# Optimization experiments

Measured on AMD Instinct MI355X. Metric: run time of the kernel, lower is better.

## Reference

```python
import jax, jax.numpy as jnp
import numpy as np

N_QUBITS = 12
N_LAYERS = 3
HID = 16
IN_DIM = 6
BATCH = 4096
C64 = jnp.complex64


def _ry(t):
    c = jnp.cos(t / 2).astype(C64)
    s = jnp.sin(t / 2).astype(C64)
    return jnp.stack([jnp.stack([c, -s], -1), jnp.stack([s, c], -1)], -2)


def _rx(t):
    c = jnp.cos(t / 2).astype(C64)
    s = jnp.sin(t / 2).astype(C64)
    js = 1j * s
    return jnp.stack([jnp.stack([c, -js], -1), jnp.stack([-js, c], -1)], -2)


def _rz(t):
    e = jnp.exp(-1j * t.astype(C64) / 2)
    z = jnp.zeros_like(e)
    return jnp.stack([jnp.stack([e, z], -1), jnp.stack([z, jnp.conj(e)], -1)], -2)


def _apply_1q(state, U, wire):
    # state: (B,) + (2,)*n ; U: (2,2) shared or (B,2,2) per-sample
    s = jnp.moveaxis(state, wire + 1, 1)
    if U.ndim == 2:
        s = jnp.einsum('ij,bj...->bi...', U, s)
    else:
        s = jnp.einsum('bij,bj...->bi...', U, s)
    return jnp.moveaxis(s, 1, wire + 1)


def _cnot(state, c, t):
    ax_c = c + 1
    s0 = jnp.take(state, 0, axis=ax_c)
    s1 = jnp.take(state, 1, axis=ax_c)
    t_ax = t + 1 if t < c else t  # target axis after removing control axis
    s1 = jnp.flip(s1, axis=t_ax)  # X on target when control=1
    return jnp.stack([s0, s1], axis=ax_c)


def _quantum(angles, qparams):
    # angles: (B, n_qubits) angle-encoding RY rotations; qparams: (L, n, 3)
    B = angles.shape[0]
    n = N_QUBITS
    state = jnp.zeros((B,) + (2,) * n, C64).at[(slice(None),) + (0,) * n].set(1.0)
    for i in range(n):
        state = _apply_1q(state, _ry(angles[:, i]), i)
    for l in range(N_LAYERS):
        for i in range(n):
            # RX then RY then RZ on wire i -> fused 2x2
            U = _rz(qparams[l, i, 2]) @ _ry(qparams[l, i, 1]) @ _rx(qparams[l, i, 0])
            state = _apply_1q(state, U, i)
        for i in range(n - 1):
            state = _cnot(state, i, i + 1)
        if n > 2:
            state = _cnot(state, n - 1, 0)
    p = state.real ** 2 + state.imag ** 2  # (B,) + (2,)*n
    evs = []
    for i in range(n):
        axes = tuple(a for a in range(1, n + 1) if a != i + 1)
        pi = p.sum(axes)  # (B, 2)
        evs.append(pi[:, 0] - pi[:, 1])
    return jnp.stack(evs, axis=1)  # (B, n) PauliZ expvals


def setup_inputs() -> dict:
    key = jax.random.key(0)
    ks = jax.random.split(key, 14)
    w = lambda k, shape: jax.random.normal(k, shape, jnp.float32) * 0.1
    return {
        'x': jax.random.normal(ks[0], (BATCH, IN_DIM), jnp.float32),
        'W1': w(ks[1], (HID, IN_DIM)), 'b1': w(ks[2], (HID,)),
        'W2': w(ks[3], (HID, HID)), 'b2': w(ks[4], (HID,)),
        'W3': w(ks[5], (N_QUBITS, HID)), 'b3': w(ks[6], (N_QUBITS,)),
        'qparams': w(ks[7], (N_LAYERS, N_QUBITS, 3)),
        'P1': w(ks[8], (HID, N_QUBITS)), 'c1': w(ks[9], (HID,)),
        'P2': w(ks[10], (8, HID)), 'c2': w(ks[11], (8,)),
        'P3': w(ks[12], (1, 8)), 'c3': w(ks[13], (1,)),
    }


def reference(x, W1, b1, W2, b2, W3, b3, qparams, P1, c1, P2, c2, P3, c3):
    # classical preprocessor (dropout = identity at inference)
    h = jax.nn.relu(x @ W1.T + b1)
    h = jax.nn.relu(h @ W2.T + b2)
    angles = h @ W3.T + b3  # (B, n_qubits)
    q = _quantum(angles, qparams)  # (B, n_qubits)
    # classical postprocessor
    o = jax.nn.relu(q @ P1.T + c1)
    o = jax.nn.relu(o @ P2.T + c2)
    o = jax.nn.sigmoid(o @ P3.T + c3)
    return o.squeeze(-1)  # (B,)
```

## Files before the change

kernel.cpp:

```cpp
#include <hip/hip_runtime.h>
#include <stdint.h>

#define NQ   12
#define DIM  4096
#define TPB  256

typedef float   v2f   __attribute__((ext_vector_type(2)));
typedef float   v4f   __attribute__((ext_vector_type(4)));
typedef float   f32x4 __attribute__((ext_vector_type(4)));
typedef _Float16 v2h  __attribute__((ext_vector_type(2)));
typedef _Float16 f16x8 __attribute__((ext_vector_type(8)));
typedef uint32_t u32x4 __attribute__((ext_vector_type(4)));

struct PassP {
  uint16_t v[4];
  uint16_t m[4];
  uint16_t td[4];
  uint8_t  np[8];
  uint8_t  wire[4];
  uint8_t  layer;
  uint8_t  pad[3];
};
struct ROC {
  uint16_t mask[12];
  uint8_t  bin[12];
};

constexpr int chbit(uint32_t x) { int b = -1; for (int i = 0; i < 32; ++i) if ((x >> i) & 1u) b = i; return b; }

constexpr void bmm(uint32_t* C, const uint32_t* A, const uint32_t* B) {
  for (int i = 0; i < NQ; ++i) {
    uint32_t r = 0;
    for (int j = 0; j < NQ; ++j) if ((A[i] >> j) & 1u) r ^= B[j];
    C[i] = r;
  }
}
constexpr void binv(const uint32_t* M, uint32_t* Inv) {
  uint32_t A[NQ] = {}, I[NQ] = {};
  for (int i = 0; i < NQ; ++i) { A[i] = M[i]; I[i] = 1u << i; }
  for (int c = 0; c < NQ; ++c) {
    int piv = -1;
    for (int r = c; r < NQ; ++r) if ((A[r] >> c) & 1u) { piv = r; break; }
    if (piv < 0) continue;
    uint32_t ta = A[c]; A[c] = A[piv]; A[piv] = ta;
    uint32_t ti = I[c]; I[c] = I[piv]; I[piv] = ti;
    for (int r = 0; r < NQ; ++r)
      if (r != c && ((A[r] >> c) & 1u)) { A[r] ^= A[c]; I[r] ^= I[c]; }
  }
  for (int i = 0; i < NQ; ++i) Inv[i] = I[i];
}

constexpr int rank5(const uint32_t* cols, int n) {
  uint32_t rows[5] = {}; int rnk = 0;
  for (int q = 0; q < n; ++q) {
    uint32_t x = cols[q] & 31u;
    for (int bit = 4; bit >= 0; --bit) {
      if (!((x >> bit) & 1u)) continue;
      if (rows[bit]) { x ^= rows[bit]; }
      else { rows[bit] = x; ++rnk; break; }
    }
  }
  return rnk;
}
constexpr int penalty(int r) {
  return r >= 5 ? 0 : r == 4 ? 58 : r == 3 ? 194 : r == 2 ? 469 : 1100;
}

constexpr PassP make_pass(int p) {
  PassP pp{};
  uint32_t A[NQ] = {}; A[0] = 0xFFEu;
  for (int i = 1; i < NQ; ++i) A[i] = (1u << (i + 1)) - 1u;
  uint32_t A2[NQ] = {}, Ai[NQ] = {}, A2i[NQ] = {};
  bmm(A2, A, A);
  binv(A, Ai); binv(A2, A2i);

  const int L = (p < 3) ? 1 : 2;
  const int wb = (p % 3) * 4;
  const uint32_t* M  = (L == 1) ? A  : A2;
  const uint32_t* Mi = (L == 1) ? Ai : A2i;
  uint32_t v0[4] = {}, m0[4] = {};
  for (int i = 0; i < 4; ++i) {
    int w = wb + i; uint32_t col = 0;
    for (int r = 0; r < NQ; ++r) col |= ((Mi[r] >> w) & 1u) << r;
    v0[i] = col; m0[i] = M[w];
  }
  uint32_t Bc[NQ] = {};
  for (int b = 0; b < NQ; ++b) {
    uint32_t col = 1u << b;
    for (int i = 0; i < 4; ++i) if ((m0[i] >> b) & 1u) col ^= v0[i];
    Bc[b] = col;
  }
  uint32_t redv[4] = {}; int pbit[4] = {}; uint32_t pivmask = 0;
  for (int i = 0; i < 4; ++i) {
    redv[i] = v0[i];
    for (int k2 = 0; k2 < i; ++k2) if ((redv[i] >> pbit[k2]) & 1u) redv[i] ^= redv[k2];
    pbit[i] = chbit(redv[i]); pivmask |= 1u << pbit[i];
  }
  uint8_t np0[8] = {}; int nc = 0;
  for (int b = 0; b < NQ; ++b) if (!((pivmask >> b) & 1u)) np0[nc++] = (uint8_t)b;

  int bestCost = 1 << 30;
  int bsel[4] = {0, 1, 2, 3}; int bperm[4] = {0, 1, 2, 3};
  for (int a = 0; a < 8; ++a) for (int b = a + 1; b < 8; ++b)
  for (int c = b + 1; c < 8; ++c) for (int d = c + 1; d < 8; ++d) {
    uint32_t jc[4] = {Bc[np0[a]], Bc[np0[b]], Bc[np0[c]], Bc[np0[d]]};
    int prk[4][4] = {};
    for (int i = 0; i < 4; ++i)
      for (int j = i + 1; j < 4; ++j) {
        uint32_t sp[6] = {jc[0], jc[1], jc[2], jc[3], v0[i], v0[j]};
        prk[i][j] = prk[j][i] = rank5(sp, 6);
      }
    for (int pa = 0; pa < 4; ++pa) for (int pb2 = 0; pb2 < 4; ++pb2) {
      if (pb2 == pa) continue;
      for (int pc = 0; pc < 4; ++pc) {
        if (pc == pa || pc == pb2) continue;
        const int pd = 6 - pa - pb2 - pc;
        const int cost = penalty(prk[pc][pd]) + penalty(prk[pb2][pc]);
        if (cost < bestCost) {
          bestCost = cost;
          bsel[0] = a; bsel[1] = b; bsel[2] = c; bsel[3] = d;
          bperm[0] = pa; bperm[1] = pb2; bperm[2] = pc; bperm[3] = pd;
        }
      }
    }
  }
  int rem[4] = {}; int rc2 = 0;
  for (int q = 0; q < 8; ++q)
    if (q != bsel[0] && q != bsel[1] && q != bsel[2] && q != bsel[3]) rem[rc2++] = q;

  uint8_t npn[8] = {};
  npn[0] = np0[bsel[0]]; npn[1] = np0[bsel[1]];
  npn[2] = np0[bsel[2]]; npn[3] = np0[bsel[3]];
  npn[4] = np0[rem[0]]; npn[5] = np0[rem[1]];
  npn[6] = np0[rem[2]]; npn[7] = np0[rem[3]];
  for (int q = 0; q < 8; ++q) pp.np[q] = npn[q];
  for (int i = 0; i < 4; ++i) {
    pp.v[i] = (uint16_t)v0[bperm[i]];
    pp.m[i] = (uint16_t)m0[bperm[i]];
    pp.wire[i] = (uint8_t)(wb + bperm[i]);
  }
  pp.td[0] = 0;
  pp.td[1] = (uint16_t)Bc[npn[4]];
  pp.td[2] = (uint16_t)Bc[npn[5]];
  pp.td[3] = (uint16_t)(Bc[npn[4]] ^ Bc[npn[5]]);
  pp.layer = (uint8_t)L;
  return pp;
}

constexpr PassP kp0 = make_pass(0);
constexpr PassP kp1 = make_pass(1);
constexpr PassP kp2 = make_pass(2);
constexpr PassP kp3 = make_pass(3);
constexpr PassP kp4 = make_pass(4);
constexpr PassP kp5 = make_pass(5);

template<int P>
constexpr PassP pget() {
  if constexpr (P == 0) return kp0;
  else if constexpr (P == 1) return kp1;
  else if constexpr (P == 2) return kp2;
  else if constexpr (P == 3) return kp3;
  else if constexpr (P == 4) return kp4;
  else return kp5;
}

constexpr ROC make_ro() {
  ROC r{};
  uint32_t A[NQ] = {}; A[0] = 0xFFEu;
  for (int i = 1; i < NQ; ++i) A[i] = (1u << (i + 1)) - 1u;
  uint32_t A2[NQ] = {}, A3[NQ] = {};
  bmm(A2, A, A); bmm(A3, A2, A);
  for (int i = 0; i < NQ; ++i) r.mask[i] = (uint16_t)A3[i];
  for (int i = 0; i < NQ; ++i) {
    uint32_t b = 0;
    b |= (uint32_t)(__builtin_popcount(A3[i] & (uint32_t)kp5.v[0]) & 1) << 0;
    b |= (uint32_t)(__builtin_popcount(A3[i] & (uint32_t)kp5.v[3]) & 1) << 1;
    b |= (uint32_t)(__builtin_popcount(A3[i] & (uint32_t)kp5.td[1]) & 1) << 2;
    b |= (uint32_t)(__builtin_popcount(A3[i] & (uint32_t)kp5.td[2]) & 1) << 3;
    r.bin[i] = (uint8_t)b;
  }
  return r;
}
constexpr ROC roc = make_ro();

__device__ __forceinline__ v2f cmulf(v2f a, v2f b) {
  return (v2f){a.x * b.x - a.y * b.y, a.x * b.y + a.y * b.x};
}
__device__ __forceinline__ uint32_t f2h2(float a, float b) {
  return __builtin_bit_cast(uint32_t, __builtin_amdgcn_cvt_pkrtz(a, b));
}
__device__ __forceinline__ uint32_t pk_rtn(float a, float b) {
  v2h h = {(_Float16)a, (_Float16)b};
  return __builtin_bit_cast(uint32_t, h);
}

__device__ __forceinline__ void build_u(const float* __restrict__ qp, int l, int w, float U[8]) {
  float p0 = qp[(l * 12 + w) * 3 + 0];
  float p1 = qp[(l * 12 + w) * 3 + 1];
  float p2 = qp[(l * 12 + w) * 3 + 2];
  float cx, sx, cy, sy, cz, sz;
  sincosf(0.5f * p0, &sx, &cx);
  sincosf(0.5f * p1, &sy, &cy);
  sincosf(0.5f * p2, &sz, &cz);
  float M00x =  cy * cx, M00y =  sy * sx;
  float M01x = -sy * cx, M01y = -cy * sx;
  float M10x =  sy * cx, M10y = -cy * sx;
  float M11x =  cy * cx, M11y = -sy * sx;
  U[0] = cz * M00x + sz * M00y; U[1] = cz * M00y - sz * M00x;
  U[2] = cz * M01x + sz * M01y; U[3] = cz * M01y - sz * M01x;
  U[4] = cz * M10x - sz * M10y; U[5] = cz * M10y + sz * M10x;
  U[6] = cz * M11x - sz * M11y; U[7] = cz * M11y + sz * M11x;
}

__device__ __forceinline__ int am_col(int c, int i) {
  return ((((c >> 2) ^ ((i >> 1) & 3)) << 2) | (c & 3));
}

template<int P>
__device__ __forceinline__ void build_am(uint32_t (*Am2)[32][16],
                                         const v2f (*gg)[12][4], int t) {
  constexpr PassP pp = pget<P>();
  const int r_ = t >> 4, c_ = t & 15;
  v2f e = (v2f){1.f, 0.f};
  #pragma unroll
  for (int i = 0; i < 4; ++i) {
    v2f u = gg[pp.layer - 1][pp.wire[i]][(((r_ >> i) & 1) << 1) | ((c_ >> i) & 1)];
    e = cmulf(e, u);
  }
  const int ra = 2 * r_, rb = 2 * r_ + 1;
  Am2[P & 1][ra][am_col(c_, ra)] = pk_rtn(e.x, -e.y);
  Am2[P & 1][rb][am_col(c_, rb)] = pk_rtn(e.y, e.x);
}

template<int P, bool LAST>
__device__ __forceinline__ void do_pass(uint32_t* st, uint32_t (*Am2)[32][16],
                                        const v2f (*gg)[12][4], int t, float* ev) {
  constexpr PassP pp = pget<P>();
  const int lane = t & 63;
  const int wv   = t >> 6;
  const int g    = lane >> 4;
  f16x8 a0, a1;
  {
    const int li = lane & 15;
    const int q0 = g ^ ((li >> 1) & 3);
    a0 = __builtin_bit_cast(f16x8, *reinterpret_cast<const u32x4*>(&Am2[P & 1][li][q0 * 4]));
    const int i1 = 16 + li;
    const int q1 = g ^ ((i1 >> 1) & 3);
    a1 = __builtin_bit_cast(f16x8, *reinterpret_cast<const u32x4*>(&Am2[P & 1][i1][q1 * 4]));
  }
  const int t6 = (lane & 15) | (wv << 6);
  int rep = 0;
  #pragma unroll
  for (int k = 0; k < 8; ++k) rep |= ((t6 >> k) & 1) << pp.np[k];
  int base = rep;
  #pragma unroll
  for (int i = 0; i < 4; ++i)
    if (__popc(pp.m[i] & rep) & 1) base ^= pp.v[i];
  const int cgr = ((g & 1) ? pp.v[2] : 0) ^ ((g & 2) ? pp.v[3] : 0);
  const int cgw = ((g & 1) ? pp.v[1] : 0) ^ ((g & 2) ? pp.v[2] : 0);
  float pr[16];
  const f32x4 z = {0.f, 0.f, 0.f, 0.f};
  #pragma unroll
  for (int T = 0; T < 4; ++T) {
    const int bT = base ^ pp.td[T];
    const int ra = bT ^ cgr;
    u32x4 braw = { st[ra], st[ra ^ pp.v[0]], st[ra ^ pp.v[1]],
                   st[ra ^ (pp.v[0] ^ pp.v[1])] };
    f16x8 bf = __builtin_bit_cast(f16x8, braw);
    f32x4 c0 = __builtin_amdgcn_mfma_f32_16x16x32_f16(a0, bf, z, 0, 0, 0);
    f32x4 c1 = __builtin_amdgcn_mfma_f32_16x16x32_f16(a1, bf, z, 0, 0, 0);
    if constexpr (!LAST) {
      const int wa = bT ^ cgw;
      st[wa]                       = f2h2(c0.x, c0.y);
      st[wa ^ pp.v[0]]             = f2h2(c0.z, c0.w);
      st[wa ^ pp.v[3]]             = f2h2(c1.x, c1.y);
      st[wa ^ (pp.v[3] ^ pp.v[0])] = f2h2(c1.z, c1.w);
    } else {
      const int nb = ((T & 1) << 2) | ((T >> 1) << 3);
      pr[nb]     = c0.x * c0.x + c0.y * c0.y;
      pr[nb | 1] = c0.z * c0.z + c0.w * c0.w;
      pr[nb | 2] = c1.x * c1.x + c1.y * c1.y;
      pr[nb | 3] = c1.z * c1.z + c1.w * c1.w;
    }
  }
  if constexpr (P < 5) build_am<P + 1>(Am2, gg, t);
  if constexpr (LAST) {
    #pragma unroll
    for (int gs = 1; gs < 16; gs <<= 1) {
      #pragma unroll
      for (int j = 0; j < 16; ++j) {
        if (j & gs) continue;
        float u = pr[j], w2 = pr[j | gs];
        pr[j] = u + w2; pr[j | gs] = u - w2;
      }
    }
    const int baseL = base ^ cgw;
    #pragma unroll
    for (int i = 0; i < NQ; ++i) {
      float h = pr[roc.bin[i]];
      int s = (__popc(roc.mask[i] & baseL) & 1) << 31;
      ev[i] = __int_as_float(__float_as_int(h) ^ s);
    }
  }
}

__global__ __launch_bounds__(TPB, 7) void hqc_kernel(
    const float* __restrict__ x,  const float* __restrict__ W1, const float* __restrict__ b1,
    const float* __restrict__ W2, const float* __restrict__ b2,
    const float* __restrict__ W3, const float* __restrict__ b3,
    const float* __restrict__ qp, const float* __restrict__ P1, const float* __restrict__ c1,
    const float* __restrict__ P2, const float* __restrict__ c2,
    const float* __restrict__ P3, const float* __restrict__ c3,
    float* __restrict__ out)
{
  __shared__ uint32_t st[DIM];
  __shared__ __align__(16) uint32_t Am2[2][32][16];
  __shared__ v2f  gg[2][12][4];
  __shared__ v4f  gpk0[12][2];
  __shared__ float red[4][NQ];

  const int s    = blockIdx.x;
  const int t    = threadIdx.x;
  const int lane = t & 63;
  const int wv   = t >> 6;

  if (wv == 0) {
    if (lane < 16) {
      float a = b1[lane];
      #pragma unroll
      for (int k = 0; k < 6; ++k) a = fmaf(W1[lane * 6 + k], x[s * 6 + k], a);
      float h1 = fmaxf(a, 0.f);
      float a2 = b2[lane];
      #pragma unroll
      for (int k = 0; k < 16; ++k) a2 = fmaf(W2[lane * 16 + k], __shfl(h1, k, 64), a2);
      float h2 = fmaxf(a2, 0.f);
      const int lw = (lane < NQ) ? lane : 0;
      float a3 = b3[lw];
      #pragma unroll
      for (int k = 0; k < 16; ++k) a3 = fmaf(W3[lw * 16 + k], __shfl(h2, k, 64), a3);
      if (lane < NQ) {
        float U[8]; build_u(qp, 0, lane, U);
        float ca, sa; sincosf(0.5f * a3, &sa, &ca);
        float c0x = U[0] * ca + U[2] * sa, c0y = U[1] * ca + U[3] * sa;
        float c1x = U[4] * ca + U[6] * sa, c1y = U[5] * ca + U[7] * sa;
        gpk0[lane][0] = (v4f){c0x, c0x, -c0y, c0y};
        gpk0[lane][1] = (v4f){c1x, c1x, -c1y, c1y};
      }
    }
  } else if (wv <= 2) {
    if (lane < NQ) {
      float U[8]; build_u(qp, wv, lane, U);
      gg[wv - 1][lane][0] = (v2f){U[0], U[1]};
      gg[wv - 1][lane][1] = (v2f){U[2], U[3]};
      gg[wv - 1][lane][2] = (v2f){U[4], U[5]};
      gg[wv - 1][lane][3] = (v2f){U[6], U[7]};
    }
  }
  __syncthreads();

  build_am<0>(Am2, gg, t);
  {
    v2f acc = (v2f){1.f, 0.f};
    #pragma unroll
    for (int i = 0; i < 8; ++i) {
      v4f gk = gpk0[i][(t >> i) & 1];
      acc = gk.xy * acc + gk.zw * acc.yx;
    }
    v2f l16[16];
    l16[0] = acc;
    #pragma unroll
    for (int i = 0; i < 4; ++i) {
      v4f g0 = gpk0[8 + i][0], g1 = gpk0[8 + i][1];
      #pragma unroll
      for (int j = 0; j < (1 << i); ++j) {
        v2f a = l16[j];
        l16[j | (1 << i)] = g1.xy * a + g1.zw * a.yx;
        l16[j]            = g0.xy * a + g0.zw * a.yx;
      }
    }
    #pragma unroll
    for (int j = 0; j < 16; ++j) st[t | (j << 8)] = f2h2(l16[j].x, l16[j].y);
  }
  __syncthreads();

  float ev[NQ];
  do_pass<0, false>(st, Am2, gg, t, ev); __syncthreads();
  do_pass<1, false>(st, Am2, gg, t, ev); __syncthreads();
  do_pass<2, false>(st, Am2, gg, t, ev); __syncthreads();
  do_pass<3, false>(st, Am2, gg, t, ev); __syncthreads();
  do_pass<4, false>(st, Am2, gg, t, ev); __syncthreads();
  do_pass<5, true >(st, Am2, gg, t, ev);

  #pragma unroll
  for (int off = 32; off >= 1; off >>= 1) {
    #pragma unroll
    for (int i = 0; i < NQ; ++i) ev[i] += __shfl_xor(ev[i], off, 64);
  }
  if (lane == 0) {
    #pragma unroll
    for (int i = 0; i < NQ; ++i) red[wv][i] = ev[i];
  }
  __syncthreads();

  if (wv == 0 && lane < 16) {
    float q = (lane < NQ)
      ? (red[0][lane] + red[1][lane] + red[2][lane] + red[3][lane])
      : 0.f;
    float a = c1[lane];
    #pragma unroll
    for (int j = 0; j < NQ; ++j) a = fmaf(P1[lane * NQ + j], __shfl(q, j, 64), a);
    float o1 = fmaxf(a, 0.f);
    float a2 = c2[lane & 7];
    #pragma unroll
    for (int j = 0; j < 16; ++j) a2 = fmaf(P2[(lane & 7) * 16 + j], __shfl(o1, j, 64), a2);
    float o2 = fmaxf(a2, 0.f);
    float a3 = c3[0];
    #pragma unroll
    for (int j = 0; j < 8; ++j) a3 = fmaf(P3[j], __shfl(o2, j, 64), a3);
    if (lane == 0) out[s] = 1.f / (1.f + expf(-a3));
  }
}

extern "C" void kernel_launch(void* const* d_in, const int* in_sizes, int n_in,
                              void* d_out, int out_size, void* d_ws, size_t ws_size,
                              hipStream_t stream) {
  (void)in_sizes; (void)n_in; (void)d_ws; (void)ws_size;
  hqc_kernel<<<out_size, TPB, 0, stream>>>(
      (const float*)d_in[0],  (const float*)d_in[1],  (const float*)d_in[2],
      (const float*)d_in[3],  (const float*)d_in[4],  (const float*)d_in[5],
      (const float*)d_in[6],  (const float*)d_in[7],  (const float*)d_in[8],
      (const float*)d_in[9],  (const float*)d_in[10], (const float*)d_in[11],
      (const float*)d_in[12], (const float*)d_in[13],
      (float*)d_out);
}
```

Measured before the change: 54.36 us.

## Precompute batch-independent gate matrices in a prep kernel and prefetch from global

Moves construction of the fused gate MFMA operand matrices and the layer-0 unitaries into a separate single-block prep kernel that writes them to workspace. The main kernel now loads each pass's A operands from global memory into registers, prefetching one pass ahead, rather than rebuilding them per block in shared memory with sincos work. This removes redundant per-block trig and LDS traffic and frees shared memory, which allows raising the launch-bounds occupancy hint from 7 to 8. In exchange it adds an extra kernel launch and keeps more operand registers live.

```diff
diff --git a/kernel.cpp b/kernel.cpp
--- a/kernel.cpp
+++ b/kernel.cpp
@@ -217,8 +217,8 @@
 }
 
 template<int P>
-__device__ __forceinline__ void build_am(uint32_t (*Am2)[32][16],
-                                         const v2f (*gg)[12][4], int t) {
+__device__ __forceinline__ void build_am_g(uint32_t* __restrict__ Am_g,
+                                           const v2f (*gg)[12][4], int t) {
   constexpr PassP pp = pget<P>();
   const int r_ = t >> 4, c_ = t & 15;
   v2f e = (v2f){1.f, 0.f};
@@ -228,26 +228,44 @@
     e = cmulf(e, u);
   }
   const int ra = 2 * r_, rb = 2 * r_ + 1;
-  Am2[P & 1][ra][am_col(c_, ra)] = pk_rtn(e.x, -e.y);
-  Am2[P & 1][rb][am_col(c_, rb)] = pk_rtn(e.y, e.x);
+  Am_g[P * 512 + ra * 16 + am_col(c_, ra)] = pk_rtn(e.x, -e.y);
+  Am_g[P * 512 + rb * 16 + am_col(c_, rb)] = pk_rtn(e.y, e.x);
+}
+
+__global__ __launch_bounds__(256) void prep_kernel(const float* __restrict__ qp,
+                                                   uint32_t* __restrict__ Am_g,
+                                                   float* __restrict__ U0_g) {
+  __shared__ v2f gg[2][12][4];
+  const int t = threadIdx.x;
+  if (t < 24) {
+    const int L = t / 12 + 1, w = t % 12;
+    float U[8]; build_u(qp, L, w, U);
+    gg[L - 1][w][0] = (v2f){U[0], U[1]};
+    gg[L - 1][w][1] = (v2f){U[2], U[3]};
+    gg[L - 1][w][2] = (v2f){U[4], U[5]};
+    gg[L - 1][w][3] = (v2f){U[6], U[7]};
+  } else if (t >= 32 && t < 44) {
+    const int w = t - 32;
+    float U[8]; build_u(qp, 0, w, U);
+    #pragma unroll
+    for (int k = 0; k < 8; ++k) U0_g[w * 8 + k] = U[k];
+  }
+  __syncthreads();
+  build_am_g<0>(Am_g, gg, t);
+  build_am_g<1>(Am_g, gg, t);
+  build_am_g<2>(Am_g, gg, t);
+  build_am_g<3>(Am_g, gg, t);
+  build_am_g<4>(Am_g, gg, t);
+  build_am_g<5>(Am_g, gg, t);
 }
 
 template<int P, bool LAST>
-__device__ __forceinline__ void do_pass(uint32_t* st, uint32_t (*Am2)[32][16],
-                                        const v2f (*gg)[12][4], int t, float* ev) {
+__device__ __forceinline__ void do_pass(uint32_t* st, f16x8 a0, f16x8 a1,
+                                        int t, float* ev) {
   constexpr PassP pp = pget<P>();
   const int lane = t & 63;
   const int wv   = t >> 6;
   const int g    = lane >> 4;
-  f16x8 a0, a1;
-  {
-    const int li = lane & 15;
-    const int q0 = g ^ ((li >> 1) & 3);
-    a0 = __builtin_bit_cast(f16x8, *reinterpret_cast<const u32x4*>(&Am2[P & 1][li][q0 * 4]));
-    const int i1 = 16 + li;
-    const int q1 = g ^ ((i1 >> 1) & 3);
-    a1 = __builtin_bit_cast(f16x8, *reinterpret_cast<const u32x4*>(&Am2[P & 1][i1][q1 * 4]));
-  }
   const int t6 = (lane & 15) | (wv << 6);
   int rep = 0;
   #pragma unroll
@@ -283,7 +301,6 @@
       pr[nb | 3] = c1.z * c1.z + c1.w * c1.w;
     }
   }
-  if constexpr (P < 5) build_am<P + 1>(Am2, gg, t);
   if constexpr (LAST) {
     #pragma unroll
     for (int gs = 1; gs < 16; gs <<= 1) {
@@ -304,18 +321,26 @@
   }
 }
 
-__global__ __launch_bounds__(TPB, 7) void hqc_kernel(
+#define LDA(P, A0, A1) {                                                        \
+  const int li_ = lane & 15;                                                    \
+  const int q_  = g ^ ((li_ >> 1) & 3);                                         \
+  A0 = __builtin_bit_cast(f16x8,                                                \
+      *reinterpret_cast<const u32x4*>(Am_g + (P) * 512 + li_ * 16 + q_ * 4));   \
+  A1 = __builtin_bit_cast(f16x8,                                                \
+      *reinterpret_cast<const u32x4*>(Am_g + (P) * 512 + (li_ + 16) * 16 + q_ * 4)); \
+}
+
+__global__ __launch_bounds__(TPB, 8) void hqc_kernel(
     const float* __restrict__ x,  const float* __restrict__ W1, const float* __restrict__ b1,
     const float* __restrict__ W2, const float* __restrict__ b2,
     const float* __restrict__ W3, const float* __restrict__ b3,
-    const float* __restrict__ qp, const float* __restrict__ P1, const float* __restrict__ c1,
+    const float* __restrict__ P1, const float* __restrict__ c1,
     const float* __restrict__ P2, const float* __restrict__ c2,
     const float* __restrict__ P3, const float* __restrict__ c3,
+    const uint32_t* __restrict__ Am_g, const float* __restrict__ U0_g,
     float* __restrict__ out)
 {
   __shared__ uint32_t st[DIM];
-  __shared__ __align__(16) uint32_t Am2[2][32][16];
-  __shared__ v2f  gg[2][12][4];
   __shared__ v4f  gpk0[12][2];
   __shared__ float red[4][NQ];
 
@@ -323,42 +348,35 @@
   const int t    = threadIdx.x;
   const int lane = t & 63;
   const int wv   = t >> 6;
-
-  if (wv == 0) {
-    if (lane < 16) {
-      float a = b1[lane];
-      #pragma unroll
-      for (int k = 0; k < 6; ++k) a = fmaf(W1[lane * 6 + k], x[s * 6 + k], a);
-      float h1 = fmaxf(a, 0.f);
-      float a2 = b2[lane];
-      #pragma unroll
-      for (int k = 0; k < 16; ++k) a2 = fmaf(W2[lane * 16 + k], __shfl(h1, k, 64), a2);
-      float h2 = fmaxf(a2, 0.f);
-      const int lw = (lane < NQ) ? lane : 0;
-      float a3 = b3[lw];
-      #pragma unroll
-      for (int k = 0; k < 16; ++k) a3 = fmaf(W3[lw * 16 + k], __shfl(h2, k, 64), a3);
-      if (lane < NQ) {
-        float U[8]; build_u(qp, 0, lane, U);
-        float ca, sa; sincosf(0.5f * a3, &sa, &ca);
-        float c0x = U[0] * ca + U[2] * sa, c0y = U[1] * ca + U[3] * sa;
-        float c1x = U[4] * ca + U[6] * sa, c1y = U[5] * ca + U[7] * sa;
-        gpk0[lane][0] = (v4f){c0x, c0x, -c0y, c0y};
-        gpk0[lane][1] = (v4f){c1x, c1x, -c1y, c1y};
-      }
-    }
-  } else if (wv <= 2) {
+  const int g    = lane >> 4;
+
+  f16x8 a0c, a1c, a0n, a1n;
+  LDA(0, a0c, a1c)
+
+  if (wv == 0 && lane < 16) {
+    float a = b1[lane];
+    #pragma unroll
+    for (int k = 0; k < 6; ++k) a = fmaf(W1[lane * 6 + k], x[s * 6 + k], a);
+    float h1 = fmaxf(a, 0.f);
+    float a2 = b2[lane];
+    #pragma unroll
+    for (int k = 0; k < 16; ++k) a2 = fmaf(W2[lane * 16 + k], __shfl(h1, k, 64), a2);
+    float h2 = fmaxf(a2, 0.f);
+    const int lw = (lane < NQ) ? lane : 0;
+    float a3 = b3[lw];
+    #pragma unroll
+    for (int k = 0; k < 16; ++k) a3 = fmaf(W3[lw * 16 + k], __shfl(h2, k, 64), a3);
     if (lane < NQ) {
-      float U[8]; build_u(qp, wv, lane, U);
-      gg[wv - 1][lane][0] = (v2f){U[0], U[1]};
-      gg[wv - 1][lane][1] = (v2f){U[2], U[3]};
-      gg[wv - 1][lane][2] = (v2f){U[4], U[5]};
-      gg[wv - 1][lane][3] = (v2f){U[6], U[7]};
+      const float* u = U0_g + lane * 8;
+      float ca, sa; sincosf(0.5f * a3, &sa, &ca);
+      float c0x = u[0] * ca + u[2] * sa, c0y = u[1] * ca + u[3] * sa;
+      float c1x = u[4] * ca + u[6] * sa, c1y = u[5] * ca + u[7] * sa;
+      gpk0[lane][0] = (v4f){c0x, c0x, -c0y, c0y};
+      gpk0[lane][1] = (v4f){c1x, c1x, -c1y, c1y};
     }
   }
   __syncthreads();
 
-  build_am<0>(Am2, gg, t);
   {
     v2f acc = (v2f){1.f, 0.f};
     #pragma unroll
@@ -384,12 +402,18 @@
   __syncthreads();
 
   float ev[NQ];
-  do_pass<0, false>(st, Am2, gg, t, ev); __syncthreads();
-  do_pass<1, false>(st, Am2, gg, t, ev); __syncthreads();
-  do_pass<2, false>(st, Am2, gg, t, ev); __syncthreads();
-  do_pass<3, false>(st, Am2, gg, t, ev); __syncthreads();
-  do_pass<4, false>(st, Am2, gg, t, ev); __syncthreads();
-  do_pass<5, true >(st, Am2, gg, t, ev);
+  LDA(1, a0n, a1n)
+  do_pass<0, false>(st, a0c, a1c, t, ev); __syncthreads();
+  a0c = a0n; a1c = a1n; LDA(2, a0n, a1n)
+  do_pass<1, false>(st, a0c, a1c, t, ev); __syncthreads();
+  a0c = a0n; a1c = a1n; LDA(3, a0n, a1n)
+  do_pass<2, false>(st, a0c, a1c, t, ev); __syncthreads();
+  a0c = a0n; a1c = a1n; LDA(4, a0n, a1n)
+  do_pass<3, false>(st, a0c, a1c, t, ev); __syncthreads();
+  a0c = a0n; a1c = a1n; LDA(5, a0n, a1n)
+  do_pass<4, false>(st, a0c, a1c, t, ev); __syncthreads();
+  a0c = a0n; a1c = a1n;
+  do_pass<5, true >(st, a0c, a1c, t, ev);
 
   #pragma unroll
   for (int off = 32; off >= 1; off >>= 1) {
@@ -424,12 +448,18 @@
 extern "C" void kernel_launch(void* const* d_in, const int* in_sizes, int n_in,
                               void* d_out, int out_size, void* d_ws, size_t ws_size,
                               hipStream_t stream) {
-  (void)in_sizes; (void)n_in; (void)d_ws; (void)ws_size;
+  (void)in_sizes; (void)n_in; (void)ws_size;
+  uint32_t* Am_g = (uint32_t*)d_ws;
+  float*    U0_g = (float*)((char*)d_ws + 6 * 512 * 4);
+  const float* qp = (const float*)d_in[7];
+  prep_kernel<<<1, 256, 0, stream>>>(qp, Am_g, U0_g);
   hqc_kernel<<<out_size, TPB, 0, stream>>>(
       (const float*)d_in[0],  (const float*)d_in[1],  (const float*)d_in[2],
       (const float*)d_in[3],  (const float*)d_in[4],  (const float*)d_in[5],
-      (const float*)d_in[6],  (const float*)d_in[7],  (const float*)d_in[8],
-      (const float*)d_in[9],  (const float*)d_in[10], (const float*)d_in[11],
+      (const float*)d_in[6],
+      (const float*)d_in[8],  (const float*)d_in[9],
+      (const float*)d_in[10], (const float*)d_in[11],
       (const float*)d_in[12], (const float*)d_in[13],
+      Am_g, U0_g,
       (float*)d_out);
 }
```

After: 56.37 us. +3.7%, slower.
